# Performance work log

Hardware: AMD Instinct MI355X
Metric: run time of the kernel (lower is better)

Reference implementation:

```python
import jax, jax.numpy as jnp
import numpy as np

H = 128   # hidden dim (all hidden_* params)
B = 256   # number of compound graphs in batch
NG = 4000  # number of compound groups (masked-out comp nodes)
NA = 10000  # number of anchors

LRELU = lambda x: jax.nn.leaky_relu(x, 0.1)
seg_sum = jax.ops.segment_sum


def seg_softmax(s, seg, n):
    # scatter_softmax over segments keyed by destination node
    m = jax.ops.segment_max(s, seg, num_segments=n)
    e = jnp.exp(s - m[seg])
    d = seg_sum(e, seg, num_segments=n)
    return e / d[seg]


def gru_cell(x, h, Wih, Whh, bih, bhh):
    # torch.nn.GRUCell semantics
    gi = x @ Wih.T + bih
    gh = h @ Whh.T + bhh
    ir, iz, inn = jnp.split(gi, 3, axis=-1)
    hr, hz, hn = jnp.split(gh, 3, axis=-1)
    r = jax.nn.sigmoid(ir + hr)
    z = jax.nn.sigmoid(iz + hz)
    n = jnp.tanh(inn + r * hn)
    return (1.0 - z) * n + z * h


def conv_stack(x, src, dst, Ws, bs, Wout, bout, n):
    # AtomConv/AnchorConv stack with dense-concat skip and output projection
    feats = [x]
    h = x
    for W, b in zip(Ws, bs):
        h = LRELU(seg_sum(h[src], dst, num_segments=n) @ W + b)
        feats.append(h)
    return LRELU(jnp.concatenate(feats, -1) @ Wout + bout)


def _forward(vert_x, site_x, masf_x, prot_edge_attr, prom_edge_attr,
             W_emb, b_emb,
             gwm_W_main, gwm_W_s2m, gwm_W_gate_main, gwm_b_gate_main,
             gwm_W_q, gwm_W_k, gwm_W_merge, gwm_W_gate_super, gwm_b_gate_super,
             gru_m_Wih, gru_m_Whh, gru_m_bih, gru_m_bhh,
             gru_s_Wih, gru_s_Whh, gru_s_bih, gru_s_bhh,
             W_site0, b_site0, W_site1, b_site1, W_site_out, b_site_out,
             W_masf0, b_masf0, W_masf1, b_masf1, W_masf_out, b_masf_out,
             W_anch0, b_anch0, W_anch1, b_anch1, W_anch_out, b_anch_out,
             W_dsite, b_dsite, W_dcomp, b_dcomp,
             vert_src, vert_dst, vert_batch, comp_src, comp_dst,
             site_src, site_dst, masf_src, masf_dst,
             prot_src, prot_dst, prom_src, prom_dst, anch_src, anch_dst,
             idx_ag_a, idx_ag_g, idx_aa_0, idx_aa_1, idx_gg_0, idx_gg_1):
    Nv = vert_x.shape[0]
    Ns = site_x.shape[0]
    Nm = masf_x.shape[0]
    # --- GraphConv_module: vertex embedding + super-node init ---
    vert = LRELU(vert_x @ W_emb + b_emb)
    supe = seg_sum(vert, vert_batch, num_segments=B)
    inv_sqrt_h = np.float32(1.0 / np.sqrt(H))
    # --- GWM iterations (shared GRU_main / GRU_super) ---
    for t in range(gwm_W_main.shape[0]):
        agg = seg_sum(vert[vert_src], vert_dst, num_segments=Nv)  # neighbor sum
        h_main = LRELU(agg @ gwm_W_main[t])
        trans = LRELU(supe @ gwm_W_s2m[t])[vert_batch]  # super -> main
        z = jax.nn.sigmoid(jnp.concatenate([h_main, trans], -1) @ gwm_W_gate_main[t] + gwm_b_gate_main[t])
        vert = gru_cell(z * h_main + (1.0 - z) * trans, vert,
                        gru_m_Wih, gru_m_Whh, gru_m_bih, gru_m_bhh)
        # main -> super attention (k_head = 1)
        q = (supe @ gwm_W_q[t])[vert_batch]
        k = vert @ gwm_W_k[t]
        score = jnp.sum(q * k, -1, keepdims=True) * inv_sqrt_h  # [Nv,1]
        attn = seg_softmax(score, vert_batch, B)
        pooled = seg_sum(attn * vert, vert_batch, num_segments=B)
        m_sup = LRELU(pooled @ gwm_W_merge[t])
        zs = jax.nn.sigmoid(jnp.concatenate([m_sup, supe], -1) @ gwm_W_gate_super[t] + gwm_b_gate_super[t])
        supe = gru_cell(zs * m_sup + (1.0 - zs) * supe, supe,
                        gru_s_Wih, gru_s_Whh, gru_s_bih, gru_s_bhh)
    # --- Group_module: uniform edge softmax (softmax of ones == 1/deg) ---
    w_g = seg_softmax(jnp.zeros((comp_src.shape[0], 1), vert.dtype), comp_dst, NG)
    group = seg_sum(w_g * vert[comp_src], comp_dst, num_segments=NG)  # [NG,H]
    # --- AtomConv_module / MasfConv_module ---
    site_out = conv_stack(site_x, site_src, site_dst, [W_site0, W_site1],
                          [b_site0, b_site1], W_site_out, b_site_out, Ns)
    masf_out = conv_stack(masf_x, masf_src, masf_dst, [W_masf0, W_masf1],
                          [b_masf0, b_masf1], W_masf_out, b_masf_out, Nm)
    # --- Anchor_module (UpwardConv with scatter_softmax(6 - dist) weights) ---
    # fill_anchor_graph's padded scatter + gather is fused into direct indexing
    w_p = seg_softmax(6.0 - prot_edge_attr, prot_dst, NA)
    anchor_atom = seg_sum(w_p * site_out[prot_src], prot_dst, num_segments=NA)
    w_m = seg_softmax(6.0 - prom_edge_attr, prom_dst, NA)
    anchor_masf = seg_sum(w_m * masf_out[prom_src], prom_dst, num_segments=NA)
    # --- AnchorAnchor_module (Affsrc == 'all': concat atom/masif anchor feats) ---
    anch = jnp.concatenate([anchor_atom, anchor_masf], -1)  # [NA,2H]
    anch_out = conv_stack(anch, anch_src, anch_dst, [W_anch0, W_anch1],
                          [b_anch0, b_anch1], W_anch_out, b_anch_out, NA)
    # --- Distance_pred_module ---
    pa = LRELU(anch_out @ W_dsite + b_dsite)
    pg = LRELU(group @ W_dcomp + b_dcomp)
    eps = np.float32(1e-6)  # torch.pairwise_distance eps
    pd = lambda a, b: jnp.sqrt(jnp.sum((a - b + eps) ** 2, -1, keepdims=True))
    ag = pd(pa[idx_ag_a], pg[idx_ag_g])
    aa = pd(pa[idx_aa_0], pa[idx_aa_1])
    gg = pd(pg[idx_gg_0], pg[idx_gg_1])
    return jnp.concatenate([ag, aa, gg], 0)  # [Pag+Paa+Pgg, 1]


def setup_inputs():
    key = jax.random.key(0)
    ks = iter(jax.random.split(key, 100))
    f32 = jnp.float32

    def nrm(shape, s=0.05):
        return jax.random.normal(next(ks), shape, f32) * s

    def ri(n, hi):
        return jax.random.randint(next(ks), (n,), 0, hi, dtype=jnp.int32)

    def zeros(*shape):
        return jnp.zeros(shape, f32)

    Nv, Ev, Ec = 20000, 80000, 40000
    Ns, Es = 80000, 320000
    Nm, Em = 80000, 320000
    Ep, Ea = 160000, 80000
    Pag, Paa, Pgg = 200000, 100000, 50000
    FV, Fs, Fm, D = 82, 256, 320, 2
    inp = {}
    inp["vert_x"] = nrm((Nv, FV), 1.0)
    inp["site_x"] = nrm((Ns, Fs), 1.0)
    inp["masf_x"] = nrm((Nm, Fm), 1.0)
    inp["prot_edge_attr"] = jax.random.uniform(next(ks), (Ep, 1), f32) * 6.0
    inp["prom_edge_attr"] = jax.random.uniform(next(ks), (Ep, 1), f32) * 6.0
    inp["vert_src"] = ri(Ev, Nv); inp["vert_dst"] = ri(Ev, Nv)
    inp["vert_batch"] = jnp.sort(ri(Nv, B))
    inp["comp_src"] = ri(Ec, Nv); inp["comp_dst"] = ri(Ec, NG)
    inp["site_src"] = ri(Es, Ns); inp["site_dst"] = ri(Es, Ns)
    inp["masf_src"] = ri(Em, Nm); inp["masf_dst"] = ri(Em, Nm)
    inp["prot_src"] = ri(Ep, Ns); inp["prot_dst"] = ri(Ep, NA)
    inp["prom_src"] = ri(Ep, Nm); inp["prom_dst"] = ri(Ep, NA)
    inp["anch_src"] = ri(Ea, NA); inp["anch_dst"] = ri(Ea, NA)
    inp["idx_ag_a"] = ri(Pag, NA); inp["idx_ag_g"] = ri(Pag, NG)
    inp["idx_aa_0"] = ri(Paa, NA); inp["idx_aa_1"] = ri(Paa, NA)
    inp["idx_gg_0"] = ri(Pgg, NG); inp["idx_gg_1"] = ri(Pgg, NG)
    inp["W_emb"] = nrm((FV, H)); inp["b_emb"] = zeros(H)
    inp["gwm_W_main"] = nrm((D, H, H)); inp["gwm_W_s2m"] = nrm((D, H, H))
    inp["gwm_W_gate_main"] = nrm((D, 2 * H, H)); inp["gwm_b_gate_main"] = zeros(D, H)
    inp["gwm_W_q"] = nrm((D, H, H)); inp["gwm_W_k"] = nrm((D, H, H))
    inp["gwm_W_merge"] = nrm((D, H, H))
    inp["gwm_W_gate_super"] = nrm((D, 2 * H, H)); inp["gwm_b_gate_super"] = zeros(D, H)
    for p in ["m", "s"]:
        inp["gru_%s_Wih" % p] = nrm((3 * H, H)); inp["gru_%s_Whh" % p] = nrm((3 * H, H))
        inp["gru_%s_bih" % p] = zeros(3 * H); inp["gru_%s_bhh" % p] = zeros(3 * H)
    inp["W_site0"] = nrm((Fs, H)); inp["b_site0"] = zeros(H)
    inp["W_site1"] = nrm((H, H)); inp["b_site1"] = zeros(H)
    inp["W_site_out"] = nrm((Fs + 2 * H, H)); inp["b_site_out"] = zeros(H)
    inp["W_masf0"] = nrm((Fm, H)); inp["b_masf0"] = zeros(H)
    inp["W_masf1"] = nrm((H, H)); inp["b_masf1"] = zeros(H)
    inp["W_masf_out"] = nrm((Fm + 2 * H, H)); inp["b_masf_out"] = zeros(H)
    inp["W_anch0"] = nrm((2 * H, H)); inp["b_anch0"] = zeros(H)
    inp["W_anch1"] = nrm((H, H)); inp["b_anch1"] = zeros(H)
    inp["W_anch_out"] = nrm((4 * H, H)); inp["b_anch_out"] = zeros(H)
    inp["W_dsite"] = nrm((H, H)); inp["b_dsite"] = zeros(H)
    inp["W_dcomp"] = nrm((H, H)); inp["b_dcomp"] = zeros(H)
    return inp


def reference(vert_x, site_x, masf_x, prot_edge_attr, prom_edge_attr,
              W_emb, b_emb,
              gwm_W_main, gwm_W_s2m, gwm_W_gate_main, gwm_b_gate_main,
              gwm_W_q, gwm_W_k, gwm_W_merge, gwm_W_gate_super, gwm_b_gate_super,
              gru_m_Wih, gru_m_Whh, gru_m_bih, gru_m_bhh,
              gru_s_Wih, gru_s_Whh, gru_s_bih, gru_s_bhh,
              W_site0, b_site0, W_site1, b_site1, W_site_out, b_site_out,
              W_masf0, b_masf0, W_masf1, b_masf1, W_masf_out, b_masf_out,
              W_anch0, b_anch0, W_anch1, b_anch1, W_anch_out, b_anch_out,
              W_dsite, b_dsite, W_dcomp, b_dcomp,
              vert_src, vert_dst, vert_batch, comp_src, comp_dst,
              site_src, site_dst, masf_src, masf_dst,
              prot_src, prot_dst, prom_src, prom_dst, anch_src, anch_dst,
              idx_ag_a, idx_ag_g, idx_aa_0, idx_aa_1, idx_gg_0, idx_gg_1):
    return _forward(vert_x, site_x, masf_x, prot_edge_attr, prom_edge_attr,
                    W_emb, b_emb,
                    gwm_W_main, gwm_W_s2m, gwm_W_gate_main, gwm_b_gate_main,
                    gwm_W_q, gwm_W_k, gwm_W_merge, gwm_W_gate_super, gwm_b_gate_super,
                    gru_m_Wih, gru_m_Whh, gru_m_bih, gru_m_bhh,
                    gru_s_Wih, gru_s_Whh, gru_s_bih, gru_s_bhh,
                    W_site0, b_site0, W_site1, b_site1, W_site_out, b_site_out,
                    W_masf0, b_masf0, W_masf1, b_masf1, W_masf_out, b_masf_out,
                    W_anch0, b_anch0, W_anch1, b_anch1, W_anch_out, b_anch_out,
                    W_dsite, b_dsite, W_dcomp, b_dcomp,
                    vert_src, vert_dst, vert_batch, comp_src, comp_dst,
                    site_src, site_dst, masf_src, masf_dst,
                    prot_src, prot_dst, prom_src, prom_dst, anch_src, anch_dst,
                    idx_ag_a, idx_ag_g, idx_aa_0, idx_aa_1, idx_gg_0, idx_gg_1)
```

## Files before the change

### kernel.cpp

```cpp
#include <hip/hip_runtime.h>
#include <math.h>

#define HD 128

typedef __bf16 bf16x8 __attribute__((ext_vector_type(8)));
typedef unsigned short u16x8 __attribute__((ext_vector_type(8)));
typedef float f32x4 __attribute__((ext_vector_type(4)));

__device__ __forceinline__ unsigned short f2bf(float f) {
    unsigned u = __float_as_uint(f);
    unsigned r = u + 0x7FFFu + ((u >> 16) & 1u);
    return (unsigned short)(r >> 16);
}

#define MAXW 32
struct WDesc { const float* src; unsigned short* dst; int K, N, Kpad, tr; };
struct WBatch { WDesc d[MAXW]; };

__global__ void convert_weights(WBatch wb)
{
    WDesc d = wb.d[blockIdx.y];
    long total = (long)d.N * d.Kpad;
    long i = (long)blockIdx.x * 256 + threadIdx.x;
    if (i >= total) return;
    int n = (int)(i / d.Kpad), k = (int)(i % d.Kpad);
    float v = 0.f;
    if (k < d.K) v = d.tr ? d.src[(size_t)k * d.N + n] : d.src[(size_t)n * d.K + k];
    d.dst[i] = f2bf(v);
}

__global__ __launch_bounds__(256)
void gemm_mfma(const float* __restrict__ A0, const float* __restrict__ A1,
               const float* __restrict__ A2, int K0, int K1, int K2,
               int lda0, int lda1, int lda2,
               const unsigned short* __restrict__ WT, int Kpad,
               const float* __restrict__ bias, float* __restrict__ C,
               int M, int N, int act,
               const float* __restrict__ G1, const float* __restrict__ G2)
{
    __shared__ __align__(16) unsigned short sA[2][64][40];
    __shared__ __align__(16) unsigned short sW[2][128][40];

    const int tid = threadIdx.x;
    const int lane = tid & 63, w = tid >> 6;
    const int mBase = blockIdx.x * 64;
    const int nBase = blockIdx.y * 128;
    const int Ktot = K0 + K1 + K2;
    const int colb = w * 32;
    const int c16 = lane & 15, g = lane >> 4;

    f32x4 acc[4][2];
#pragma unroll
    for (int i = 0; i < 4; ++i)
#pragma unroll
        for (int j = 0; j < 2; ++j) acc[i][j] = (f32x4){0.f, 0.f, 0.f, 0.f};

    const int kTiles = (Ktot + 31) / 32;

    auto loadTile = [&](int kt, float f[8], u16x8& h0, u16x8& h1) {
        const int k0g = kt * 32;
        const float* Ab; int lda, kloc, segK;
        if (k0g < K0)           { Ab = A0; lda = lda0; kloc = k0g;           segK = K0; }
        else if (k0g < K0 + K1) { Ab = A1; lda = lda1; kloc = k0g - K0;      segK = K1; }
        else                    { Ab = A2; lda = lda2; kloc = k0g - K0 - K1; segK = K2; }
        int row = tid >> 2, kq = (tid & 3) * 8;
        int gr = mBase + row;
        if (gr < M && ((lda & 3) == 0) && (kloc + kq + 8 <= segK)) {
            const float* ap = Ab + (size_t)gr * lda + kloc + kq;
            float4 v0 = *(const float4*)ap, v1 = *(const float4*)(ap + 4);
            f[0] = v0.x; f[1] = v0.y; f[2] = v0.z; f[3] = v0.w;
            f[4] = v1.x; f[5] = v1.y; f[6] = v1.z; f[7] = v1.w;
        } else {
#pragma unroll
            for (int i = 0; i < 8; ++i) {
                int kk = kloc + kq + i;
                f[i] = (gr < M && kk < segK) ? Ab[(size_t)gr * lda + kk] : 0.f;
            }
        }
        int col = tid >> 1, kh = (tid & 1) * 16;
        const unsigned short* wp = WT + (size_t)(nBase + col) * Kpad + k0g + kh;
        h0 = *(const u16x8*)wp;
        h1 = *(const u16x8*)(wp + 8);
    };
    auto stageWrite = [&](int buf, const float f[8], u16x8 h0, u16x8 h1) {
        int row = tid >> 2, kq = (tid & 3) * 8;
        u16x8 h;
#pragma unroll
        for (int i = 0; i < 8; ++i) h[i] = f2bf(f[i]);
        *(u16x8*)&sA[buf][row][kq] = h;
        int col = tid >> 1, kh = (tid & 1) * 16;
        *(u16x8*)&sW[buf][col][kh] = h0;
        *(u16x8*)&sW[buf][col][kh + 8] = h1;
    };
    auto compute = [&](int buf) {
        bf16x8 bfr0 = __builtin_bit_cast(bf16x8, *(const u16x8*)&sW[buf][colb + c16][g * 8]);
        bf16x8 bfr1 = __builtin_bit_cast(bf16x8, *(const u16x8*)&sW[buf][colb + 16 + c16][g * 8]);
#pragma unroll
        for (int rf = 0; rf < 4; ++rf) {
            bf16x8 af = __builtin_bit_cast(bf16x8, *(const u16x8*)&sA[buf][rf * 16 + c16][g * 8]);
            acc[rf][0] = __builtin_amdgcn_mfma_f32_16x16x32_bf16(af, bfr0, acc[rf][0], 0, 0, 0);
            acc[rf][1] = __builtin_amdgcn_mfma_f32_16x16x32_bf16(af, bfr1, acc[rf][1], 0, 0, 0);
        }
    };

    float fN[8]; u16x8 hN0, hN1;
    {
        float fC[8]; u16x8 hC0, hC1;
        loadTile(0, fC, hC0, hC1);
        stageWrite(0, fC, hC0, hC1);
        if (kTiles > 1) loadTile(1, fN, hN0, hN1);
    }
    asm volatile("s_waitcnt lgkmcnt(0)" ::: "memory");
    __builtin_amdgcn_s_barrier();

    int cur = 0;
#pragma unroll 2
    for (int kt = 0; kt < kTiles; ++kt) {
        float fP[8]; u16x8 hP0, hP1;
        const bool pf = (kt + 2 < kTiles);
        if (pf) loadTile(kt + 2, fP, hP0, hP1);
        compute(cur);
        if (kt + 1 < kTiles) stageWrite(cur ^ 1, fN, hN0, hN1);
        asm volatile("s_waitcnt lgkmcnt(0)" ::: "memory");
        __builtin_amdgcn_s_barrier();
        if (pf) {
#pragma unroll
            for (int i = 0; i < 8; ++i) fN[i] = fP[i];
            hN0 = hP0; hN1 = hP1;
        }
        cur ^= 1;
    }

#pragma unroll
    for (int cf = 0; cf < 2; ++cf) {
        int col = nBase + colb + cf * 16 + c16;
        float bb = bias ? bias[col] : 0.f;
#pragma unroll
        for (int rf = 0; rf < 4; ++rf) {
            int r0 = mBase + rf * 16 + g * 4;
#pragma unroll
            for (int r = 0; r < 4; ++r) {
                int gr = r0 + r;
                if (gr >= M) continue;
                size_t o = (size_t)gr * N + col;
                float v = acc[rf][cf][r] + bb;
                if (act == 1) v = v > 0.f ? v : 0.1f * v;
                else if (act == 2) v = 1.f / (1.f + expf(-v));
                else if (act == 3) {
                    float z = 1.f / (1.f + expf(-v));
                    v = z * G1[o] + (1.f - z) * G2[o];
                }
                C[o] = v;
            }
        }
    }
}

__global__ void hist_k(int* __restrict__ cnt, const int* __restrict__ dst, int E)
{
    int i = blockIdx.x * 256 + threadIdx.x;
    if (i < E) atomicAdd(&cnt[dst[i]], 1);
}

#define SCB 4096

__global__ __launch_bounds__(256)
void scan_sums(const int* __restrict__ cnt, int n, int* __restrict__ bsum)
{
    __shared__ int red[256];
    int t = threadIdx.x;
    int base = blockIdx.x * SCB + t * 16;
    int s = 0;
#pragma unroll
    for (int i = 0; i < 16; ++i) { int idx = base + i; if (idx < n) s += cnt[idx]; }
    red[t] = s; __syncthreads();
    for (int st = 128; st > 0; st >>= 1) {
        if (t < st) red[t] += red[t + st];
        __syncthreads();
    }
    if (t == 0) bsum[blockIdx.x] = red[0];
}

__global__ void scan_bsum(int* __restrict__ bsum, int nb)
{
    if (threadIdx.x == 0) {
        int run = 0;
        for (int i = 0; i < nb; ++i) { int v = bsum[i]; bsum[i] = run; run += v; }
    }
}

__global__ __launch_bounds__(256)
void scan_write(const int* __restrict__ cnt, int n, const int* __restrict__ bsum,
                int* __restrict__ rp)
{
    __shared__ int a0[256], a1[256];
    int t = threadIdx.x;
    int base = blockIdx.x * SCB + t * 16;
    int v[16]; int s = 0;
#pragma unroll
    for (int i = 0; i < 16; ++i) { int idx = base + i; v[i] = (idx < n) ? cnt[idx] : 0; s += v[i]; }
    a0[t] = s; __syncthreads();
    int* cur = a0; int* nxt = a1;
    for (int st = 1; st < 256; st <<= 1) {
        int val = cur[t] + ((t >= st) ? cur[t - st] : 0);
        nxt[t] = val; __syncthreads();
        int* tmp = cur; cur = nxt; nxt = tmp;
    }
    int run = bsum[blockIdx.x] + (t > 0 ? cur[t - 1] : 0);
#pragma unroll
    for (int i = 0; i < 16; ++i) {
        int idx = base + i;
        if (idx < n) {
            rp[idx] = run; run += v[i];
            if (idx == n - 1) rp[n] = run;
        }
    }
}

__global__ void fill_k(int* __restrict__ eidx, int* __restrict__ cursor,
                       const int* __restrict__ dst, int E)
{
    int i = blockIdx.x * 256 + threadIdx.x;
    if (i < E) eidx[atomicAdd(&cursor[dst[i]], 1)] = i;
}

__global__ __launch_bounds__(256)
void seg_gather(float* __restrict__ out, const float* __restrict__ X,
                const int* __restrict__ rowptr, const int* __restrict__ eidx,
                const int* __restrict__ src, const float* __restrict__ wattr,
                const float* __restrict__ bias, int n, int ostride, int ooff,
                int act, int mode)
{
    int d = blockIdx.x * 4 + (threadIdx.x >> 6);
    if (d >= n) return;
    int lane = threadIdx.x & 63;
    int lo = rowptr[d], hi = rowptr[d + 1];
    float w0 = 1.f, mx = 0.f, iden = 0.f;
    if (mode == 2) w0 = (hi > lo) ? 1.f / (float)(hi - lo) : 0.f;
    if (mode == 3) {
        float mxl = -1e30f;
        for (int base = lo; base < hi; base += 64) {
            int i = base + lane;
            if (i < hi) mxl = fmaxf(mxl, 6.f - wattr[eidx[i]]);
        }
#pragma unroll
        for (int o = 32; o; o >>= 1) mxl = fmaxf(mxl, __shfl_xor(mxl, o));
        mx = mxl;
        float dl = 0.f;
        for (int base = lo; base < hi; base += 64) {
            int i = base + lane;
            if (i < hi) dl += expf(6.f - wattr[eidx[i]] - mx);
        }
#pragma unroll
        for (int o = 32; o; o >>= 1) dl += __shfl_xor(dl, o);
        iden = 1.f / dl;
    }

    float ax = 0.f, ay = 0.f;
    int i = lo;
    for (; i + 4 <= hi; i += 4) {
        int e0 = eidx[i], e1 = eidx[i + 1], e2 = eidx[i + 2], e3 = eidx[i + 3];
        int s0 = src ? src[e0] : e0, s1 = src ? src[e1] : e1;
        int s2 = src ? src[e2] : e2, s3 = src ? src[e3] : e3;
        float w0v, w1v, w2v, w3v;
        if (mode == 0) { w0v = w1v = w2v = w3v = 1.f; }
        else if (mode == 1) { w0v = wattr[e0]; w1v = wattr[e1]; w2v = wattr[e2]; w3v = wattr[e3]; }
        else if (mode == 2) { w0v = w1v = w2v = w3v = w0; }
        else {
            w0v = expf(6.f - wattr[e0] - mx) * iden;
            w1v = expf(6.f - wattr[e1] - mx) * iden;
            w2v = expf(6.f - wattr[e2] - mx) * iden;
            w3v = expf(6.f - wattr[e3] - mx) * iden;
        }
        float2 v0 = *(const float2*)(X + (size_t)s0 * HD + 2 * lane);
        float2 v1 = *(const float2*)(X + (size_t)s1 * HD + 2 * lane);
        float2 v2 = *(const float2*)(X + (size_t)s2 * HD + 2 * lane);
        float2 v3 = *(const float2*)(X + (size_t)s3 * HD + 2 * lane);
        ax += w0v * v0.x + w1v * v1.x + w2v * v2.x + w3v * v3.x;
        ay += w0v * v0.y + w1v * v1.y + w2v * v2.y + w3v * v3.y;
    }
    for (; i < hi; ++i) {
        int e = eidx[i];
        int s = src ? src[e] : e;
        float w;
        if (mode == 0) w = 1.f;
        else if (mode == 1) w = wattr[e];
        else if (mode == 2) w = w0;
        else w = expf(6.f - wattr[e] - mx) * iden;
        float2 v = *(const float2*)(X + (size_t)s * HD + 2 * lane);
        ax += w * v.x; ay += w * v.y;
    }
    if (bias) { float2 b = *(const float2*)(bias + 2 * lane); ax += b.x; ay += b.y; }
    if (act == 1) { ax = ax > 0.f ? ax : 0.1f * ax; ay = ay > 0.f ? ay : 0.1f * ay; }
    *(float2*)(out + (size_t)d * ostride + ooff + 2 * lane) = make_float2(ax, ay);
}

__global__ __launch_bounds__(256)
void seg_softmax_csr(float* __restrict__ sc, const int* __restrict__ rowptr,
                     const int* __restrict__ eidx, int n)
{
    int d = blockIdx.x * 4 + (threadIdx.x >> 6);
    if (d >= n) return;
    int lane = threadIdx.x & 63;
    int lo = rowptr[d], hi = rowptr[d + 1];
    float mxl = -1e30f;
    for (int i = lo + lane; i < hi; i += 64) mxl = fmaxf(mxl, sc[eidx[i]]);
#pragma unroll
    for (int o = 32; o; o >>= 1) mxl = fmaxf(mxl, __shfl_xor(mxl, o));
    float dl = 0.f;
    for (int i = lo + lane; i < hi; i += 64) dl += expf(sc[eidx[i]] - mxl);
#pragma unroll
    for (int o = 32; o; o >>= 1) dl += __shfl_xor(dl, o);
    float iden = 1.f / dl;
    for (int i = lo + lane; i < hi; i += 64) {
        int v = eidx[i];
        sc[v] = expf(sc[v] - mxl) * iden;
    }
}

__global__ void gather128(float* __restrict__ out, const float* __restrict__ in,
                          const int* __restrict__ idx, int n)
{
    long i = (long)blockIdx.x * 256 + threadIdx.x;
    if (i >= (long)n * HD) return;
    int r = (int)(i >> 7), f = (int)(i & 127);
    out[i] = in[(size_t)idx[r] * HD + f];
}

__global__ void gru_gate(float* __restrict__ h, const float* __restrict__ gi,
                         const float* __restrict__ gh, int M)
{
    long i = (long)blockIdx.x * 256 + threadIdx.x;
    if (i >= (long)M * HD) return;
    int row = (int)(i >> 7), f = (int)(i & 127);
    size_t o = (size_t)row * 384 + f;
    float r = 1.f / (1.f + expf(-(gi[o] + gh[o])));
    float z = 1.f / (1.f + expf(-(gi[o + 128] + gh[o + 128])));
    float n = tanhf(gi[o + 256] + r * gh[o + 256]);
    h[i] = (1.f - z) * n + z * h[i];
}

__global__ void dot_score(float* __restrict__ sc, const float* __restrict__ kb,
                          const float* __restrict__ qs, const int* __restrict__ batch, int n)
{
    int v = blockIdx.x * 256 + threadIdx.x;
    if (v >= n) return;
    const float4* a = (const float4*)(kb + (size_t)v * HD);
    const float4* q = (const float4*)(qs + (size_t)batch[v] * HD);
    float acc = 0.f;
#pragma unroll
    for (int i = 0; i < 32; ++i) {
        float4 x = a[i], y = q[i];
        acc += x.x * y.x + x.y * y.y + x.z * y.z + x.w * y.w;
    }
    sc[v] = acc * 0.08838834764831843f;
}

__global__ void pdist_k(float* __restrict__ out, const float* __restrict__ A,
                        const float* __restrict__ Bm, const int* __restrict__ ia,
                        const int* __restrict__ ib, int P)
{
    int p = blockIdx.x * 256 + threadIdx.x;
    if (p >= P) return;
    const float4* a = (const float4*)(A + (size_t)ia[p] * HD);
    const float4* b = (const float4*)(Bm + (size_t)ib[p] * HD);
    float acc = 0.f;
#pragma unroll
    for (int i = 0; i < 32; ++i) {
        float4 x = a[i], y = b[i];
        float d0 = x.x - y.x + 1e-6f, d1 = x.y - y.y + 1e-6f;
        float d2 = x.z - y.z + 1e-6f, d3 = x.w - y.w + 1e-6f;
        acc += d0 * d0 + d1 * d1 + d2 * d2 + d3 * d3;
    }
    out[p] = sqrtf(acc);
}


static inline unsigned gupd(size_t n) { return (unsigned)((n + 255) / 256); }
static inline unsigned gup4(size_t n) { return (unsigned)((n + 3) / 4); }

struct WArena { unsigned short* p; int Kpad; };

static void gemm3s(hipStream_t st, const float* A0, int K0, const float* A1, int K1,
                   const float* A2, int K2, WArena wa, const float* bias,
                   float* C, int M, int N, int act,
                   const float* G1 = nullptr, const float* G2 = nullptr)
{
    dim3 g((M + 63) / 64, N / 128);
    hipLaunchKernelGGL(gemm_mfma, g, dim3(256), 0, st, A0, A1, A2, K0, K1, K2,
                       K0, K1, K2, wa.p, wa.Kpad, bias, C, M, N, act, G1, G2);
}
static void gemm1(hipStream_t st, const float* A, int K, WArena wa, const float* bias,
                  float* C, int M, int N, int act)
{ gemm3s(st, A, K, nullptr, 0, nullptr, 0, wa, bias, C, M, N, act); }
static void gemm2g(hipStream_t st, const float* A0, int K0, const float* A1, int K1,
                   WArena wa, const float* bias, float* C, int M, int N, int act,
                   const float* G1 = nullptr, const float* G2 = nullptr)
{ gemm3s(st, A0, K0, A1, K1, nullptr, 0, wa, bias, C, M, N, act, G1, G2); }

extern "C" void kernel_launch(void* const* d_in, const int* in_sizes, int n_in,
                              void* d_out, int out_size, void* d_ws, size_t ws_size,
                              hipStream_t stream)
{
    (void)n_in; (void)out_size;
    const float* vert_x  = (const float*)d_in[0];
    const float* site_x  = (const float*)d_in[1];
    const float* masf_x  = (const float*)d_in[2];
    const float* prot_ea = (const float*)d_in[3];
    const float* prom_ea = (const float*)d_in[4];
    const int* vert_src = (const int*)d_in[5];
    const int* vert_dst = (const int*)d_in[6];
    const int* vbatch   = (const int*)d_in[7];
    const int* comp_src = (const int*)d_in[8];
    const int* comp_dst = (const int*)d_in[9];
    const int* site_src = (const int*)d_in[10];
    const int* site_dst = (const int*)d_in[11];
    const int* masf_src = (const int*)d_in[12];
    const int* masf_dst = (const int*)d_in[13];
    const int* prot_src = (const int*)d_in[14];
    const int* prot_dst = (const int*)d_in[15];
    const int* prom_src = (const int*)d_in[16];
    const int* prom_dst = (const int*)d_in[17];
    const int* anch_src = (const int*)d_in[18];
    const int* anch_dst = (const int*)d_in[19];
    const int* ag_a = (const int*)d_in[20];
    const int* ag_g = (const int*)d_in[21];
    const int* aa0  = (const int*)d_in[22];
    const int* aa1  = (const int*)d_in[23];
    const int* gg0  = (const int*)d_in[24];
    const int* gg1  = (const int*)d_in[25];
    const float* W_emb = (const float*)d_in[26];
    const float* b_emb = (const float*)d_in[27];
    const float* gW_main = (const float*)d_in[28];
    const float* gW_s2m  = (const float*)d_in[29];
    const float* gW_gm   = (const float*)d_in[30];
    const float* gb_gm   = (const float*)d_in[31];
    const float* gW_q    = (const float*)d_in[32];
    const float* gW_k    = (const float*)d_in[33];
    const float* gW_mrg  = (const float*)d_in[34];
    const float* gW_gs   = (const float*)d_in[35];
    const float* gb_gs   = (const float*)d_in[36];
    const float* gm_Wih = (const float*)d_in[37];
    const float* gm_Whh = (const float*)d_in[38];
    const float* gm_bih = (const float*)d_in[39];
    const float* gm_bhh = (const float*)d_in[40];
    const float* gs_Wih = (const float*)d_in[41];
    const float* gs_Whh = (const float*)d_in[42];
    const float* gs_bih = (const float*)d_in[43];
    const float* gs_bhh = (const float*)d_in[44];
    const float* W_s0 = (const float*)d_in[45];
    const float* b_s0 = (const float*)d_in[46];
    const float* W_s1 = (const float*)d_in[47];
    const float* b_s1 = (const float*)d_in[48];
    const float* W_so = (const float*)d_in[49];
    const float* b_so = (const float*)d_in[50];
    const float* W_m0 = (const float*)d_in[51];
    const float* b_m0 = (const float*)d_in[52];
    const float* W_m1 = (const float*)d_in[53];
    const float* b_m1 = (const float*)d_in[54];
    const float* W_mo = (const float*)d_in[55];
    const float* b_mo = (const float*)d_in[56];
    const float* W_a0 = (const float*)d_in[57];
    const float* b_a0 = (const float*)d_in[58];
    const float* W_a1 = (const float*)d_in[59];
    const float* b_a1 = (const float*)d_in[60];
    const float* W_ao = (const float*)d_in[61];
    const float* b_ao = (const float*)d_in[62];
    const float* W_ds = (const float*)d_in[63];
    const float* b_ds = (const float*)d_in[64];
    const float* W_dc = (const float*)d_in[65];
    const float* b_dc = (const float*)d_in[66];

    const int B = 256, NG = 4000, NA = 10000, Ns = 80000, Nm = 80000;
    const int Nv = in_sizes[7];
    const int FV = in_sizes[0] / Nv;
    const int Fs = in_sizes[1] / Ns;
    const int Fm = in_sizes[2] / Nm;
    const int Ev = in_sizes[5], Ec = in_sizes[8], Es = in_sizes[10], Em = in_sizes[12];
    const int Ep = in_sizes[14], Ea = in_sizes[18];
    const int Pag = in_sizes[20], Paa = in_sizes[22], Pgg = in_sizes[24];
    const int D = in_sizes[28] / (HD * HD);

    float* ws = (float*)d_ws;
    size_t off = 0;
    auto take = [&](size_t n) { size_t o = off; off += n; return o; };
    float* vert  = ws + take((size_t)Nv * HD);
    float* supe  = ws + take((size_t)B * HD);
    float* qsup  = ws + take((size_t)B * HD);
    float* pool  = ws + take((size_t)B * HD);
    float* msup  = ws + take((size_t)B * HD);
    float* zsup  = ws + take((size_t)B * HD);
    float* gis   = ws + take((size_t)B * 3 * HD);
    float* ghs   = ws + take((size_t)B * 3 * HD);
    float* tsml  = ws + take((size_t)B * HD);
    float* grp   = ws + take((size_t)NG * HD);
    float* site_o = ws + take((size_t)Ns * HD);
    float* masf_o = ws + take((size_t)Nm * HD);
    float* anch  = ws + take((size_t)NA * 2 * HD);
    float* ah1   = ws + take((size_t)NA * HD);
    float* ah2   = ws + take((size_t)NA * HD);
    float* axw   = ws + take((size_t)NA * HD);
    float* aout  = ws + take((size_t)NA * HD);
    float* pa    = ws + take((size_t)NA * HD);
    float* pg    = ws + take((size_t)NG * HD);
    float* score = ws + take((size_t)Nv);
    const size_t NvH = (size_t)Nv * HD, NsH = (size_t)Ns * HD;
    float* T = ws + take(3 * NsH);

    const int nN[8] = {Nv, NG, Ns, Nm, NA, NA, NA, B};
    const int nE[8] = {Ev, Ec, Es, Em, Ep, Ep, Ea, Nv};
    const int* dsts[8] = {vert_dst, comp_dst, site_dst, masf_dst,
                          prot_dst, prom_dst, anch_dst, vbatch};
    int baseN[9], baseE[9];
    baseN[0] = 0; baseE[0] = 0;
    for (int g = 0; g < 8; ++g) { baseN[g + 1] = baseN[g] + nN[g]; baseE[g + 1] = baseE[g] + nE[g]; }
    const int totN = baseN[8], totE = baseE[8];

    int* ib = (int*)(ws + off);
    size_t ioff = 0;
    auto taki = [&](size_t n) { size_t o = ioff; ioff += n; return o; };
    int* cnt_all = ib + taki((size_t)totN);
    int* rp_all  = ib + taki((size_t)totN + 1);
    int* cur_all = ib + taki((size_t)totN);
    int* ei_all  = ib + taki((size_t)totE);
    int* bsum    = ib + taki((size_t)((totN + SCB - 1) / SCB) + 1);
    ioff = (ioff + 7) & ~(size_t)7;

    unsigned short* warena = (unsigned short*)(ib + ioff);
    size_t woff = 0;
    WBatch wb; int nW = 0; long maxWTot = 0;
    auto reg = [&](const float* src, int K, int N, int tr) {
        int Kpad = (K + 31) & ~31;
        unsigned short* dst = warena + woff;
        woff += (size_t)N * Kpad;
        long tot = (long)N * Kpad; if (tot > maxWTot) maxWTot = tot;
        wb.d[nW].src = src; wb.d[nW].dst = dst; wb.d[nW].K = K;
        wb.d[nW].N = N; wb.d[nW].Kpad = Kpad; wb.d[nW].tr = tr;
        ++nW;
        WArena a; a.p = dst; a.Kpad = Kpad; return a;
    };
    WArena wa_emb = reg(W_emb, FV, HD, 1);
    WArena wa_main[2], wa_s2m[2], wa_gm[2], wa_q[2], wa_k[2], wa_mrg[2], wa_gs[2];
    for (int t = 0; t < D && t < 2; ++t) {
        wa_main[t] = reg(gW_main + (size_t)t * HD * HD, HD, HD, 1);
        wa_s2m[t]  = reg(gW_s2m  + (size_t)t * HD * HD, HD, HD, 1);
        wa_gm[t]   = reg(gW_gm   + (size_t)t * 2 * HD * HD, 2 * HD, HD, 1);
        wa_q[t]    = reg(gW_q    + (size_t)t * HD * HD, HD, HD, 1);
        wa_k[t]    = reg(gW_k    + (size_t)t * HD * HD, HD, HD, 1);
        wa_mrg[t]  = reg(gW_mrg  + (size_t)t * HD * HD, HD, HD, 1);
        wa_gs[t]   = reg(gW_gs   + (size_t)t * 2 * HD * HD, 2 * HD, HD, 1);
    }
    WArena wa_mih = reg(gm_Wih, HD, 3 * HD, 0);
    WArena wa_mhh = reg(gm_Whh, HD, 3 * HD, 0);
    WArena wa_sih = reg(gs_Wih, HD, 3 * HD, 0);
    WArena wa_shh = reg(gs_Whh, HD, 3 * HD, 0);
    WArena wa_s0 = reg(W_s0, Fs, HD, 1);
    WArena wa_s1 = reg(W_s1, HD, HD, 1);
    WArena wa_so = reg(W_so, Fs + 2 * HD, HD, 1);
    WArena wa_m0 = reg(W_m0, Fm, HD, 1);
    WArena wa_m1 = reg(W_m1, HD, HD, 1);
    WArena wa_mo = reg(W_mo, Fm + 2 * HD, HD, 1);
    WArena wa_a0 = reg(W_a0, 2 * HD, HD, 1);
    WArena wa_a1 = reg(W_a1, HD, HD, 1);
    WArena wa_ao = reg(W_ao, 4 * HD, HD, 1);
    WArena wa_ds = reg(W_ds, HD, HD, 1);
    WArena wa_dc = reg(W_dc, HD, HD, 1);

    if (ws_size < off * sizeof(float) + ioff * sizeof(int) + woff * sizeof(unsigned short))
        return;

    {
        dim3 g((unsigned)((maxWTot + 255) / 256), nW);
        hipLaunchKernelGGL(convert_weights, g, dim3(256), 0, stream, wb);
    }

    hipMemsetAsync(cnt_all, 0, (size_t)totN * sizeof(int), stream);
    for (int g = 0; g < 8; ++g)
        hist_k<<<gupd((size_t)nE[g]), 256, 0, stream>>>(cnt_all + baseN[g], dsts[g], nE[g]);
    const int nScanBlocks = (totN + SCB - 1) / SCB;
    scan_sums<<<nScanBlocks, 256, 0, stream>>>(cnt_all, totN, bsum);
    scan_bsum<<<1, 64, 0, stream>>>(bsum, nScanBlocks);
    scan_write<<<nScanBlocks, 256, 0, stream>>>(cnt_all, totN, bsum, rp_all);
    hipMemcpyAsync(cur_all, rp_all, (size_t)totN * sizeof(int), hipMemcpyDeviceToDevice, stream);
    for (int g = 0; g < 8; ++g)
        fill_k<<<gupd((size_t)nE[g]), 256, 0, stream>>>(ei_all, cur_all + baseN[g], dsts[g], nE[g]);

    const int* rp_v = rp_all + baseN[0];
    const int* rp_c = rp_all + baseN[1];
    const int* rp_s = rp_all + baseN[2];
    const int* rp_m = rp_all + baseN[3];
    const int* rp_p = rp_all + baseN[4];
    const int* rp_q = rp_all + baseN[5];
    const int* rp_a = rp_all + baseN[6];
    const int* rp_b = rp_all + baseN[7];
    const int* ei = ei_all;

    gemm1(stream, vert_x, FV, wa_emb, b_emb, vert, Nv, HD, 1);
    seg_gather<<<gup4(B), 256, 0, stream>>>(supe, vert, rp_b, ei, nullptr, nullptr,
                                            nullptr, B, HD, 0, 0, 0);

    float* Ta = T;            float* Tb = T + NvH;     float* Tc = T + 2 * NvH;
    float* Td = T + 3 * NvH;  float* Te = T + 4 * NvH; float* Tf = T + 7 * NvH;
    for (int t = 0; t < D; ++t) {
        const float* bgm = gb_gm + (size_t)t * HD;
        const float* bgs = gb_gs + (size_t)t * HD;

        gemm1(stream, vert, HD, wa_main[t], nullptr, Ta, Nv, HD, 0);
        seg_gather<<<gup4((size_t)Nv), 256, 0, stream>>>(Tb, Ta, rp_v, ei, vert_src,
                                                         nullptr, nullptr, Nv, HD, 0, 1, 0);
        gemm1(stream, supe, HD, wa_s2m[t], nullptr, tsml, B, HD, 1);
        gather128<<<gupd(NvH), 256, 0, stream>>>(Tc, tsml, vbatch, Nv);
        gemm2g(stream, Tb, HD, Tc, HD, wa_gm[t], bgm, Td, Nv, HD, 3, Tb, Tc);
        gemm1(stream, Td, HD, wa_mih, gm_bih, Te, Nv, 3 * HD, 0);
        gemm1(stream, vert, HD, wa_mhh, gm_bhh, Tf, Nv, 3 * HD, 0);
        gru_gate<<<gupd(NvH), 256, 0, stream>>>(vert, Te, Tf, Nv);
        gemm1(stream, vert, HD, wa_k[t], nullptr, Ta, Nv, HD, 0);
        gemm1(stream, supe, HD, wa_q[t], nullptr, qsup, B, HD, 0);
        dot_score<<<gupd((size_t)Nv), 256, 0, stream>>>(score, Ta, qsup, vbatch, Nv);
        seg_softmax_csr<<<gup4(B), 256, 0, stream>>>(score, rp_b, ei, B);
        seg_gather<<<gup4(B), 256, 0, stream>>>(pool, vert, rp_b, ei, nullptr, score,
                                                nullptr, B, HD, 0, 0, 1);
        gemm1(stream, pool, HD, wa_mrg[t], nullptr, msup, B, HD, 1);
        gemm2g(stream, msup, HD, supe, HD, wa_gs[t], bgs, zsup, B, HD, 3, msup, supe);
        gemm1(stream, zsup, HD, wa_sih, gs_bih, gis, B, 3 * HD, 0);
        gemm1(stream, supe, HD, wa_shh, gs_bhh, ghs, B, 3 * HD, 0);
        gru_gate<<<gupd((size_t)B * HD), 256, 0, stream>>>(supe, gis, ghs, B);
    }

    seg_gather<<<gup4((size_t)NG), 256, 0, stream>>>(grp, vert, rp_c, ei, comp_src,
                                                     nullptr, nullptr, NG, HD, 0, 0, 2);

    float* T1 = T; float* T2 = T + NsH; float* T3 = T + 2 * NsH;
    gemm1(stream, site_x, Fs, wa_s0, nullptr, T1, Ns, HD, 0);
    seg_gather<<<gup4((size_t)Ns), 256, 0, stream>>>(T2, T1, rp_s, ei, site_src,
                                                     nullptr, b_s0, Ns, HD, 0, 1, 0);
    gemm1(stream, T2, HD, wa_s1, nullptr, T1, Ns, HD, 0);
    seg_gather<<<gup4((size_t)Ns), 256, 0, stream>>>(T3, T1, rp_s, ei, site_src,
                                                     nullptr, b_s1, Ns, HD, 0, 1, 0);
    gemm3s(stream, site_x, Fs, T2, HD, T3, HD, wa_so, b_so, site_o, Ns, HD, 1);

    gemm1(stream, masf_x, Fm, wa_m0, nullptr, T1, Nm, HD, 0);
    seg_gather<<<gup4((size_t)Nm), 256, 0, stream>>>(T2, T1, rp_m, ei, masf_src,
                                                     nullptr, b_m0, Nm, HD, 0, 1, 0);
    gemm1(stream, T2, HD, wa_m1, nullptr, T1, Nm, HD, 0);
    seg_gather<<<gup4((size_t)Nm), 256, 0, stream>>>(T3, T1, rp_m, ei, masf_src,
                                                     nullptr, b_m1, Nm, HD, 0, 1, 0);
    gemm3s(stream, masf_x, Fm, T2, HD, T3, HD, wa_mo, b_mo, masf_o, Nm, HD, 1);

    seg_gather<<<gup4((size_t)NA), 256, 0, stream>>>(anch, site_o, rp_p, ei, prot_src,
                                                     prot_ea, nullptr, NA, 2 * HD, 0, 0, 3);
    seg_gather<<<gup4((size_t)NA), 256, 0, stream>>>(anch, masf_o, rp_q, ei, prom_src,
                                                     prom_ea, nullptr, NA, 2 * HD, HD, 0, 3);

    gemm1(stream, anch, 2 * HD, wa_a0, nullptr, axw, NA, HD, 0);
    seg_gather<<<gup4((size_t)NA), 256, 0, stream>>>(ah1, axw, rp_a, ei, anch_src,
                                                     nullptr, b_a0, NA, HD, 0, 1, 0);
    gemm1(stream, ah1, HD, wa_a1, nullptr, axw, NA, HD, 0);
    seg_gather<<<gup4((size_t)NA), 256, 0, stream>>>(ah2, axw, rp_a, ei, anch_src,
                                                     nullptr, b_a1, NA, HD, 0, 1, 0);
    gemm3s(stream, anch, 2 * HD, ah1, HD, ah2, HD, wa_ao, b_ao, aout, NA, HD, 1);

    gemm1(stream, aout, HD, wa_ds, b_ds, pa, NA, HD, 1);
    gemm1(stream, grp, HD, wa_dc, b_dc, pg, NG, HD, 1);
    float* outp = (float*)d_out;
    pdist_k<<<gupd((size_t)Pag), 256, 0, stream>>>(outp, pa, pg, ag_a, ag_g, Pag);
    pdist_k<<<gupd((size_t)Paa), 256, 0, stream>>>(outp + Pag, pa, pa, aa0, aa1, Paa);
    pdist_k<<<gupd((size_t)Pgg), 256, 0, stream>>>(outp + Pag + Paa, pg, pg, gg0, gg1, Pgg);
}
```

Measured before the change: 1.330 ms.

## Fold key projection into query side and deepen GEMM prefetch to three tiles

The attention score previously projected every vertex through W_k (an Nv x 128 x 128 GEMM) and then took a dot product with the query. It now computes u = q·W_kᵀ once per super node (a B x 128 GEMM) and dots the raw vertex features with u, which removes the large per-vertex GEMM and its write/read of an Nv x 128 buffer. Separately, the GEMM main loop keeps global-load prefetch three tiles ahead instead of two, to hide more memory latency at the cost of extra registers, which may reduce occupancy.

```diff
diff --git a/kernel.cpp b/kernel.cpp
--- a/kernel.cpp
+++ b/kernel.cpp
@@ -103,12 +103,13 @@
         }
     };
 
-    float fN[8]; u16x8 hN0, hN1;
+    float f1[8], f2[8]; u16x8 w1a, w1b, w2a, w2b;
     {
-        float fC[8]; u16x8 hC0, hC1;
-        loadTile(0, fC, hC0, hC1);
-        stageWrite(0, fC, hC0, hC1);
-        if (kTiles > 1) loadTile(1, fN, hN0, hN1);
+        float f0[8]; u16x8 w0a, w0b;
+        loadTile(0, f0, w0a, w0b);
+        stageWrite(0, f0, w0a, w0b);
+        if (kTiles > 1) loadTile(1, f1, w1a, w1b);
+        if (kTiles > 2) loadTile(2, f2, w2a, w2b);
     }
     asm volatile("s_waitcnt lgkmcnt(0)" ::: "memory");
     __builtin_amdgcn_s_barrier();
@@ -116,17 +117,22 @@
     int cur = 0;
 #pragma unroll 2
     for (int kt = 0; kt < kTiles; ++kt) {
-        float fP[8]; u16x8 hP0, hP1;
-        const bool pf = (kt + 2 < kTiles);
-        if (pf) loadTile(kt + 2, fP, hP0, hP1);
+        float fP[8]; u16x8 wPa, wPb;
+        const bool pf = (kt + 3 < kTiles);
+        if (pf) loadTile(kt + 3, fP, wPa, wPb);
         compute(cur);
-        if (kt + 1 < kTiles) stageWrite(cur ^ 1, fN, hN0, hN1);
+        if (kt + 1 < kTiles) stageWrite(cur ^ 1, f1, w1a, w1b);
         asm volatile("s_waitcnt lgkmcnt(0)" ::: "memory");
         __builtin_amdgcn_s_barrier();
+        if (kt + 2 < kTiles) {
+#pragma unroll
+            for (int i = 0; i < 8; ++i) f1[i] = f2[i];
+            w1a = w2a; w1b = w2b;
+        }
         if (pf) {
 #pragma unroll
-            for (int i = 0; i < 8; ++i) fN[i] = fP[i];
-            hN0 = hP0; hN1 = hP1;
+            for (int i = 0; i < 8; ++i) f2[i] = fP[i];
+            w2a = wPa; w2b = wPb;
         }
         cur ^= 1;
     }
@@ -340,13 +346,13 @@
     h[i] = (1.f - z) * n + z * h[i];
 }
 
-__global__ void dot_score(float* __restrict__ sc, const float* __restrict__ kb,
-                          const float* __restrict__ qs, const int* __restrict__ batch, int n)
+__global__ void dot_score(float* __restrict__ sc, const float* __restrict__ vert,
+                          const float* __restrict__ u, const int* __restrict__ batch, int n)
 {
     int v = blockIdx.x * 256 + threadIdx.x;
     if (v >= n) return;
-    const float4* a = (const float4*)(kb + (size_t)v * HD);
-    const float4* q = (const float4*)(qs + (size_t)batch[v] * HD);
+    const float4* a = (const float4*)(vert + (size_t)v * HD);
+    const float4* q = (const float4*)(u + (size_t)batch[v] * HD);
     float acc = 0.f;
 #pragma unroll
     for (int i = 0; i < 32; ++i) {
@@ -487,6 +493,7 @@
     float* vert  = ws + take((size_t)Nv * HD);
     float* supe  = ws + take((size_t)B * HD);
     float* qsup  = ws + take((size_t)B * HD);
+    float* usup  = ws + take((size_t)B * HD);
     float* pool  = ws + take((size_t)B * HD);
     float* msup  = ws + take((size_t)B * HD);
     float* zsup  = ws + take((size_t)B * HD);
@@ -540,13 +547,13 @@
         WArena a; a.p = dst; a.Kpad = Kpad; return a;
     };
     WArena wa_emb = reg(W_emb, FV, HD, 1);
-    WArena wa_main[2], wa_s2m[2], wa_gm[2], wa_q[2], wa_k[2], wa_mrg[2], wa_gs[2];
+    WArena wa_main[2], wa_s2m[2], wa_gm[2], wa_q[2], wa_kT[2], wa_mrg[2], wa_gs[2];
     for (int t = 0; t < D && t < 2; ++t) {
         wa_main[t] = reg(gW_main + (size_t)t * HD * HD, HD, HD, 1);
         wa_s2m[t]  = reg(gW_s2m  + (size_t)t * HD * HD, HD, HD, 1);
         wa_gm[t]   = reg(gW_gm   + (size_t)t * 2 * HD * HD, 2 * HD, HD, 1);
         wa_q[t]    = reg(gW_q    + (size_t)t * HD * HD, HD, HD, 1);
-        wa_k[t]    = reg(gW_k    + (size_t)t * HD * HD, HD, HD, 1);
+        wa_kT[t]   = reg(gW_k    + (size_t)t * HD * HD, HD, HD, 0);
         wa_mrg[t]  = reg(gW_mrg  + (size_t)t * HD * HD, HD, HD, 1);
         wa_gs[t]   = reg(gW_gs   + (size_t)t * 2 * HD * HD, 2 * HD, HD, 1);
     }
@@ -614,9 +621,9 @@
         gemm1(stream, Td, HD, wa_mih, gm_bih, Te, Nv, 3 * HD, 0);
         gemm1(stream, vert, HD, wa_mhh, gm_bhh, Tf, Nv, 3 * HD, 0);
         gru_gate<<<gupd(NvH), 256, 0, stream>>>(vert, Te, Tf, Nv);
-        gemm1(stream, vert, HD, wa_k[t], nullptr, Ta, Nv, HD, 0);
         gemm1(stream, supe, HD, wa_q[t], nullptr, qsup, B, HD, 0);
-        dot_score<<<gupd((size_t)Nv), 256, 0, stream>>>(score, Ta, qsup, vbatch, Nv);
+        gemm1(stream, qsup, HD, wa_kT[t], nullptr, usup, B, HD, 0);
+        dot_score<<<gupd((size_t)Nv), 256, 0, stream>>>(score, vert, usup, vbatch, Nv);
         seg_softmax_csr<<<gup4(B), 256, 0, stream>>>(score, rp_b, ei, B);
         seg_gather<<<gup4(B), 256, 0, stream>>>(pool, vert, rp_b, ei, nullptr, score,
                                                 nullptr, B, HD, 0, 0, 1);
```

After: 1.383 ms. +4.0%, slower.

## Reassociate attention score via q·W_k^T and gather super rows inside GEMM

Applied to the files above, without the earlier changes.

The per-vertex key projection (an Nv×128×128 GEMM) is replaced by projecting the small per-graph query through W_k transposed, so the score becomes a dot of vert with a per-graph vector. The separate gather128 kernel that broadcast per-graph s2m features to every vertex is also removed. The GEMM loads the second A segment and the gate's G2 operand through a row-index array instead. This removes one large GEMM, one gather kernel and a full Nv×128 intermediate, at the cost of indirect row loads in the GEMM and a small extra B-sized GEMM.

```diff
diff --git a/kernel.cpp b/kernel.cpp
--- a/kernel.cpp
+++ b/kernel.cpp
@@ -36,7 +36,8 @@
                const unsigned short* __restrict__ WT, int Kpad,
                const float* __restrict__ bias, float* __restrict__ C,
                int M, int N, int act,
-               const float* __restrict__ G1, const float* __restrict__ G2)
+               const float* __restrict__ G1, const float* __restrict__ G2,
+               const int* __restrict__ ridx1, int g2ridx)
 {
     __shared__ __align__(16) unsigned short sA[2][64][40];
     __shared__ __align__(16) unsigned short sW[2][128][40];
@@ -59,14 +60,15 @@
 
     auto loadTile = [&](int kt, float f[8], u16x8& h0, u16x8& h1) {
         const int k0g = kt * 32;
-        const float* Ab; int lda, kloc, segK;
+        const float* Ab; int lda, kloc, segK; const int* ri = nullptr;
         if (k0g < K0)           { Ab = A0; lda = lda0; kloc = k0g;           segK = K0; }
-        else if (k0g < K0 + K1) { Ab = A1; lda = lda1; kloc = k0g - K0;      segK = K1; }
+        else if (k0g < K0 + K1) { Ab = A1; lda = lda1; kloc = k0g - K0;      segK = K1; ri = ridx1; }
         else                    { Ab = A2; lda = lda2; kloc = k0g - K0 - K1; segK = K2; }
         int row = tid >> 2, kq = (tid & 3) * 8;
         int gr = mBase + row;
+        int ar = (ri && gr < M) ? ri[gr] : gr;
         if (gr < M && ((lda & 3) == 0) && (kloc + kq + 8 <= segK)) {
-            const float* ap = Ab + (size_t)gr * lda + kloc + kq;
+            const float* ap = Ab + (size_t)ar * lda + kloc + kq;
             float4 v0 = *(const float4*)ap, v1 = *(const float4*)(ap + 4);
             f[0] = v0.x; f[1] = v0.y; f[2] = v0.z; f[3] = v0.w;
             f[4] = v1.x; f[5] = v1.y; f[6] = v1.z; f[7] = v1.w;
@@ -74,7 +76,7 @@
 #pragma unroll
             for (int i = 0; i < 8; ++i) {
                 int kk = kloc + kq + i;
-                f[i] = (gr < M && kk < segK) ? Ab[(size_t)gr * lda + kk] : 0.f;
+                f[i] = (gr < M && kk < segK) ? Ab[(size_t)ar * lda + kk] : 0.f;
             }
         }
         int col = tid >> 1, kh = (tid & 1) * 16;
@@ -148,7 +150,8 @@
                 else if (act == 2) v = 1.f / (1.f + expf(-v));
                 else if (act == 3) {
                     float z = 1.f / (1.f + expf(-v));
-                    v = z * G1[o] + (1.f - z) * G2[o];
+                    size_t o2 = g2ridx ? ((size_t)ridx1[gr] * N + col) : o;
+                    v = z * G1[o] + (1.f - z) * G2[o2];
                 }
                 C[o] = v;
             }
@@ -318,15 +321,6 @@
     }
 }
 
-__global__ void gather128(float* __restrict__ out, const float* __restrict__ in,
-                          const int* __restrict__ idx, int n)
-{
-    long i = (long)blockIdx.x * 256 + threadIdx.x;
-    if (i >= (long)n * HD) return;
-    int r = (int)(i >> 7), f = (int)(i & 127);
-    out[i] = in[(size_t)idx[r] * HD + f];
-}
-
 __global__ void gru_gate(float* __restrict__ h, const float* __restrict__ gi,
                          const float* __restrict__ gh, int M)
 {
@@ -340,13 +334,13 @@
     h[i] = (1.f - z) * n + z * h[i];
 }
 
-__global__ void dot_score(float* __restrict__ sc, const float* __restrict__ kb,
-                          const float* __restrict__ qs, const int* __restrict__ batch, int n)
+__global__ void dot_score(float* __restrict__ sc, const float* __restrict__ vert,
+                          const float* __restrict__ u, const int* __restrict__ batch, int n)
 {
     int v = blockIdx.x * 256 + threadIdx.x;
     if (v >= n) return;
-    const float4* a = (const float4*)(kb + (size_t)v * HD);
-    const float4* q = (const float4*)(qs + (size_t)batch[v] * HD);
+    const float4* a = (const float4*)(vert + (size_t)v * HD);
+    const float4* q = (const float4*)(u + (size_t)batch[v] * HD);
     float acc = 0.f;
 #pragma unroll
     for (int i = 0; i < 32; ++i) {
@@ -384,19 +378,17 @@
 static void gemm3s(hipStream_t st, const float* A0, int K0, const float* A1, int K1,
                    const float* A2, int K2, WArena wa, const float* bias,
                    float* C, int M, int N, int act,
-                   const float* G1 = nullptr, const float* G2 = nullptr)
+                   const float* G1 = nullptr, const float* G2 = nullptr,
+                   const int* ridx1 = nullptr, int g2ridx = 0)
 {
     dim3 g((M + 63) / 64, N / 128);
     hipLaunchKernelGGL(gemm_mfma, g, dim3(256), 0, st, A0, A1, A2, K0, K1, K2,
-                       K0, K1, K2, wa.p, wa.Kpad, bias, C, M, N, act, G1, G2);
+                       K0, K1, K2, wa.p, wa.Kpad, bias, C, M, N, act, G1, G2,
+                       ridx1, g2ridx);
 }
 static void gemm1(hipStream_t st, const float* A, int K, WArena wa, const float* bias,
                   float* C, int M, int N, int act)
 { gemm3s(st, A, K, nullptr, 0, nullptr, 0, wa, bias, C, M, N, act); }
-static void gemm2g(hipStream_t st, const float* A0, int K0, const float* A1, int K1,
-                   WArena wa, const float* bias, float* C, int M, int N, int act,
-                   const float* G1 = nullptr, const float* G2 = nullptr)
-{ gemm3s(st, A0, K0, A1, K1, nullptr, 0, wa, bias, C, M, N, act, G1, G2); }
 
 extern "C" void kernel_launch(void* const* d_in, const int* in_sizes, int n_in,
                               void* d_out, int out_size, void* d_ws, size_t ws_size,
@@ -487,6 +479,7 @@
     float* vert  = ws + take((size_t)Nv * HD);
     float* supe  = ws + take((size_t)B * HD);
     float* qsup  = ws + take((size_t)B * HD);
+    float* usup  = ws + take((size_t)B * HD);
     float* pool  = ws + take((size_t)B * HD);
     float* msup  = ws + take((size_t)B * HD);
     float* zsup  = ws + take((size_t)B * HD);
@@ -540,13 +533,13 @@
         WArena a; a.p = dst; a.Kpad = Kpad; return a;
     };
     WArena wa_emb = reg(W_emb, FV, HD, 1);
-    WArena wa_main[2], wa_s2m[2], wa_gm[2], wa_q[2], wa_k[2], wa_mrg[2], wa_gs[2];
+    WArena wa_main[2], wa_s2m[2], wa_gm[2], wa_q[2], wa_kT[2], wa_mrg[2], wa_gs[2];
     for (int t = 0; t < D && t < 2; ++t) {
         wa_main[t] = reg(gW_main + (size_t)t * HD * HD, HD, HD, 1);
         wa_s2m[t]  = reg(gW_s2m  + (size_t)t * HD * HD, HD, HD, 1);
         wa_gm[t]   = reg(gW_gm   + (size_t)t * 2 * HD * HD, 2 * HD, HD, 1);
         wa_q[t]    = reg(gW_q    + (size_t)t * HD * HD, HD, HD, 1);
-        wa_k[t]    = reg(gW_k    + (size_t)t * HD * HD, HD, HD, 1);
+        wa_kT[t]   = reg(gW_k    + (size_t)t * HD * HD, HD, HD, 0);
         wa_mrg[t]  = reg(gW_mrg  + (size_t)t * HD * HD, HD, HD, 1);
         wa_gs[t]   = reg(gW_gs   + (size_t)t * 2 * HD * HD, 2 * HD, HD, 1);
     }
@@ -599,7 +592,7 @@
     seg_gather<<<gup4(B), 256, 0, stream>>>(supe, vert, rp_b, ei, nullptr, nullptr,
                                             nullptr, B, HD, 0, 0, 0);
 
-    float* Ta = T;            float* Tb = T + NvH;     float* Tc = T + 2 * NvH;
+    float* Ta = T;            float* Tb = T + NvH;
     float* Td = T + 3 * NvH;  float* Te = T + 4 * NvH; float* Tf = T + 7 * NvH;
     for (int t = 0; t < D; ++t) {
         const float* bgm = gb_gm + (size_t)t * HD;
@@ -609,19 +602,20 @@
         seg_gather<<<gup4((size_t)Nv), 256, 0, stream>>>(Tb, Ta, rp_v, ei, vert_src,
                                                          nullptr, nullptr, Nv, HD, 0, 1, 0);
         gemm1(stream, supe, HD, wa_s2m[t], nullptr, tsml, B, HD, 1);
-        gather128<<<gupd(NvH), 256, 0, stream>>>(Tc, tsml, vbatch, Nv);
-        gemm2g(stream, Tb, HD, Tc, HD, wa_gm[t], bgm, Td, Nv, HD, 3, Tb, Tc);
+        gemm3s(stream, Tb, HD, tsml, HD, nullptr, 0, wa_gm[t], bgm, Td, Nv, HD, 3,
+               Tb, tsml, vbatch, 1);
         gemm1(stream, Td, HD, wa_mih, gm_bih, Te, Nv, 3 * HD, 0);
         gemm1(stream, vert, HD, wa_mhh, gm_bhh, Tf, Nv, 3 * HD, 0);
         gru_gate<<<gupd(NvH), 256, 0, stream>>>(vert, Te, Tf, Nv);
-        gemm1(stream, vert, HD, wa_k[t], nullptr, Ta, Nv, HD, 0);
         gemm1(stream, supe, HD, wa_q[t], nullptr, qsup, B, HD, 0);
-        dot_score<<<gupd((size_t)Nv), 256, 0, stream>>>(score, Ta, qsup, vbatch, Nv);
+        gemm1(stream, qsup, HD, wa_kT[t], nullptr, usup, B, HD, 0);
+        dot_score<<<gupd((size_t)Nv), 256, 0, stream>>>(score, vert, usup, vbatch, Nv);
         seg_softmax_csr<<<gup4(B), 256, 0, stream>>>(score, rp_b, ei, B);
         seg_gather<<<gup4(B), 256, 0, stream>>>(pool, vert, rp_b, ei, nullptr, score,
                                                 nullptr, B, HD, 0, 0, 1);
         gemm1(stream, pool, HD, wa_mrg[t], nullptr, msup, B, HD, 1);
-        gemm2g(stream, msup, HD, supe, HD, wa_gs[t], bgs, zsup, B, HD, 3, msup, supe);
+        gemm3s(stream, msup, HD, supe, HD, nullptr, 0, wa_gs[t], bgs, zsup, B, HD, 3,
+               msup, supe, nullptr, 0);
         gemm1(stream, zsup, HD, wa_sih, gs_bih, gis, B, 3 * HD, 0);
         gemm1(stream, supe, HD, wa_shh, gs_bhh, ghs, B, 3 * HD, 0);
         gru_gate<<<gupd((size_t)B * HD), 256, 0, stream>>>(supe, gis, ghs, B);
```

Measured after the change: 1.310 ms. No clear change (-1.4%).
